# Performance work log

Hardware: AMD Instinct MI355X
Metric: run time of the kernel (lower is better)

Reference implementation:

```python
import jax, jax.numpy as jnp
import numpy as np

B, T, D = 8, 1024, 1024
L = 512          # quantizer_latent_dim
V = 8192         # codebook_size
COMMIT = 0.25
PERP_COEF = 0.1


def _l2norm(v, axis=-1):
    return v * jax.lax.rsqrt(jnp.sum(v * v, axis=axis, keepdims=True) + 1e-12)


def _sq_dist(a, b):
    # ||a||^2 - 2 a.b + ||b||^2, a:[N,L] b:[V,L] -> [N,V]
    a2 = jnp.sum(a * a, axis=1, keepdims=True)
    b2 = jnp.sum(b * b, axis=1)[None, :]
    return a2 - 2.0 * jnp.einsum('nl,vl->nv', a, b) + b2


def setup_inputs() -> dict:
    key = jax.random.key(0)
    ks = jax.random.split(key, 4)
    x = jax.random.normal(ks[0], (B, T, D), dtype=jnp.float32)
    codebook = jax.random.normal(ks[1], (V, D), dtype=jnp.float32)
    W_in = jax.random.normal(ks[2], (D, L), dtype=jnp.float32) * (1.0 / np.sqrt(D))
    b_in = jnp.zeros((L,), dtype=jnp.float32)
    W_code = jax.random.normal(ks[3], (D, L), dtype=jnp.float32) * (1.0 / np.sqrt(D))
    b_code = jnp.zeros((L,), dtype=jnp.float32)
    return {"x": x, "codebook": codebook, "W_in": W_in, "b_in": b_in,
            "W_code": W_code, "b_code": b_code}


def _train_loss(quantized, x):
    e_latent = jnp.mean((jax.lax.stop_gradient(quantized) - x) ** 2) * COMMIT
    q_latent = jnp.mean((quantized - jax.lax.stop_gradient(x)) ** 2)
    return e_latent + q_latent


def reference(x, codebook, W_in, b_in, W_code, b_code):
    xf = x.reshape(-1, D)                                      # [N, D]
    latent_input = _l2norm(xf @ W_in + b_in)                   # [N, L]
    latent_code = _l2norm(codebook @ W_code + b_code)          # [V, L]
    sg_latent_code = jax.lax.stop_gradient(_l2norm(latent_code))
    distances = _sq_dist(latent_input, sg_latent_code).reshape(B, T, V)

    # approx_min_k with aggregate_to_topk (k = top_k_value = 1)
    idx = jax.lax.approx_min_k(distances, k=1, reduction_dimension=-1,
                               aggregate_to_topk=True)[1][..., 0]   # [B, T]
    encodings = jax.nn.one_hot(idx, V, dtype=x.dtype)          # [B, T, V]
    quantized = jnp.einsum('btv,vd->btd', encodings, codebook) # [B, T, D]

    codebook_usage = jnp.sum(jnp.sum(encodings, axis=(0, 1)) > 0) / V

    # train=True path: stop-grad quantized, straight-through estimator
    q_sg = jax.lax.stop_gradient(quantized)
    loss = _train_loss(q_sg, x)
    latent_quantized = q_sg @ W_code + b_code                  # code_to_latent(quantized)
    latent_x = x @ W_in + b_in                                 # input_to_latent(x)
    loss = loss + _train_loss(latent_quantized, latent_x)

    quantized_st = x + jax.lax.stop_gradient(q_sg - x)

    avg_probs = jnp.mean(encodings.reshape(-1, V), axis=0)
    log_perplexity = -jnp.sum(avg_probs * jnp.log(avg_probs + 1e-10))
    perplexity = jnp.exp(log_perplexity)
    loss = loss + PERP_COEF * log_perplexity

    return quantized_st, loss, perplexity, codebook_usage
```

## Files before the change

kernel.cpp:

```cpp
#include <hip/hip_runtime.h>
#include <hip/hip_bf16.h>
#include <stdint.h>

#define NTOK 8192
#define DDIM 1024
#define LDIM 512
#define VCB  8192
#define MROWS 16384

typedef unsigned long long u64;
typedef unsigned short ushort_t;
typedef unsigned char u8;
typedef float f32x4 __attribute__((ext_vector_type(4)));
typedef short s16x8 __attribute__((ext_vector_type(8)));
typedef int i32x8 __attribute__((ext_vector_type(8)));

#define OFF_AB     0ull
#define OFF_QB     0ull
#define OFF_P      ((u64)MROWS * DDIM * 2)
#define OFF_QF     (OFF_P + (u64)MROWS * LDIM * 2)
#define OFF_WT     (OFF_QF + (u64)MROWS * 512)
#define OFF_B2     (OFF_WT + (u64)2 * LDIM * DDIM * 2)
#define OFF_B2B    (OFF_B2 + (u64)VCB * 4)
#define OFF_PART   (OFF_B2B + (u64)VCB * 4)
#define OFF_HIST   (OFF_PART + (u64)NTOK * 64 * 4)
#define OFF_PARTQ  (OFF_HIST + (u64)VCB * 4)
#define OFF_PARTL  (OFF_PARTQ + (u64)NTOK * 4)

__device__ __forceinline__ unsigned key_of(float f) {
  unsigned u = __float_as_uint(f);
  return (u & 0x80000000u) ? ~u : (u | 0x80000000u);
}

__device__ __forceinline__ ushort_t f2bf(float f) {
  unsigned u = __float_as_uint(f);
  unsigned r = (u + 0x7fffu + ((u >> 16) & 1u)) >> 16;
  return (ushort_t)r;
}
__device__ __forceinline__ float bf2f(unsigned b) {
  return __uint_as_float(b << 16);
}
__device__ __forceinline__ unsigned pkbf(float a, float b) {
  __hip_bfloat162 h = __float22bfloat162_rn(make_float2(a, b));
  unsigned r;
  __builtin_memcpy(&r, &h, 4);
  return r;
}

__device__ __forceinline__ void gload_lds16(const void* g, void* l) {
  __builtin_amdgcn_global_load_lds(
      (const __attribute__((address_space(1))) unsigned int*)g,
      (__attribute__((address_space(3))) unsigned int*)l, 16, 0, 0);
}

__device__ __forceinline__ f32x4 mfma16(s16x8 a, s16x8 b, f32x4 c) {
  return __builtin_amdgcn_mfma_f32_16x16x32_bf16(a, b, c, 0, 0, 0);
}
__device__ __forceinline__ f32x4 mfma_mx(i32x8 a, i32x8 b, f32x4 c) {
  return __builtin_amdgcn_mfma_scale_f32_16x16x128_f8f6f4(
      a, b, c, 0, 0, 0, 0x7f7f7f7f, 0, 0x7f7f7f7f);
}

__global__ __launch_bounds__(256)
void k_wt(const float* __restrict__ Wi, const float* __restrict__ Wc,
          ushort_t* __restrict__ Wt, int* __restrict__ hist) {
  __shared__ float tile[32][33];
  const int tx = threadIdx.x, ty = threadIdx.y;
  const int t = ty * 32 + tx;
  const int lb = blockIdx.z * 512 + blockIdx.y * 32 + blockIdx.x;
  if (lb < 32) hist[lb * 256 + t] = 0;
  const float* W = blockIdx.z ? Wc : Wi;
  ushort_t* O = Wt + (blockIdx.z ? (size_t)LDIM * DDIM : 0);
  const int k0 = blockIdx.x * 32, n0 = blockIdx.y * 32;
#pragma unroll
  for (int i = 0; i < 4; ++i)
    tile[ty * 4 + i][tx] = W[(size_t)(k0 + ty * 4 + i) * LDIM + n0 + tx];
  __syncthreads();
#pragma unroll
  for (int i = 0; i < 4; ++i)
    O[(size_t)(n0 + ty * 4 + i) * DDIM + k0 + tx] = f2bf(tile[tx][ty * 4 + i]);
}

__global__ __launch_bounds__(256)
void k_cast(const float* __restrict__ x, const float* __restrict__ cb,
            ushort_t* __restrict__ Ab) {
  size_t i = ((size_t)blockIdx.x * 256 + threadIdx.x) * 8;
  const size_t half = (size_t)NTOK * DDIM;
  const float* src = (i < half) ? (x + i) : (cb + (i - half));
  float4 a = *(const float4*)src;
  float4 b = *(const float4*)(src + 4);
  uint4 o = make_uint4(pkbf(a.x, a.y), pkbf(a.z, a.w),
                       pkbf(b.x, b.y), pkbf(b.z, b.w));
  *(uint4*)&Ab[i] = o;
}

__global__ __launch_bounds__(256)
void k_latent(const ushort_t* __restrict__ Ab, const ushort_t* __restrict__ Wt,
              const float* __restrict__ bi, const float* __restrict__ bc,
              ushort_t* __restrict__ Pb) {
  __shared__ __align__(16) ushort_t As[128 * 32];
  __shared__ __align__(16) ushort_t Bs[128 * 32];
  const int t = threadIdx.x;
  const int wave = t >> 6, lane = t & 63;
  const int col0 = blockIdx.x * 128;
  const int m0 = blockIdx.y * 128;
  const bool isCode = (m0 >= NTOK);
  const u8* A = (const u8*)(Ab + (size_t)m0 * DDIM);
  const u8* W = (const u8*)(Wt + (isCode ? (size_t)LDIM * DDIM : 0) +
                            (size_t)col0 * DDIM);
  const float* bias = isCode ? bc : bi;

  const int srow = lane >> 2;
  const int rA = wave * 16 + srow;
  const int rB = 64 + wave * 16 + srow;
  const size_t goA = (size_t)rA * 2048 +
                     (((lane & 3) ^ (rA & 3) ^ ((rA >> 2) & 3)) << 4);
  const size_t goB = (size_t)rB * 2048 +
                     (((lane & 3) ^ (rB & 3) ^ ((rB >> 2) & 3)) << 4);
  u8* lwA0 = (u8*)As + (wave * 16) * 64;
  u8* lwA1 = (u8*)As + (64 + wave * 16) * 64;
  u8* lwB0 = (u8*)Bs + (wave * 16) * 64;
  u8* lwB1 = (u8*)Bs + (64 + wave * 16) * 64;

  const int wm = wave >> 1, wn = wave & 1;
  const int m = lane & 15, q = lane >> 4;
  const int pq = (q ^ (m & 3) ^ ((m >> 2) & 3)) * 16;
  int roffA[4], roffB[4];
#pragma unroll
  for (int i = 0; i < 4; ++i) {
    roffA[i] = (wm * 64 + i * 16 + m) * 64 + pq;
    roffB[i] = (wn * 64 + i * 16 + m) * 64 + pq;
  }

  f32x4 acc[4][4];
#pragma unroll
  for (int i = 0; i < 4; ++i)
#pragma unroll
    for (int j = 0; j < 4; ++j) acc[i][j] = (f32x4)(0.f);

  for (int it = 0; it < DDIM / 32; ++it) {
    const size_t kb = (size_t)it * 64;
    __syncthreads();
    gload_lds16(A + goA + kb, lwA0);
    gload_lds16(A + goB + kb, lwA1);
    gload_lds16(W + goA + kb, lwB0);
    gload_lds16(W + goB + kb, lwB1);
    __syncthreads();
    s16x8 af[4], bfr[4];
#pragma unroll
    for (int i = 0; i < 4; ++i)
      af[i] = *(const s16x8*)((const u8*)As + roffA[i]);
#pragma unroll
    for (int j = 0; j < 4; ++j)
      bfr[j] = *(const s16x8*)((const u8*)Bs + roffB[j]);
#pragma unroll
    for (int i = 0; i < 4; ++i)
#pragma unroll
      for (int j = 0; j < 4; ++j)
        acc[i][j] = mfma16(af[i], bfr[j], acc[i][j]);
  }

  float bv[4];
#pragma unroll
  for (int j = 0; j < 4; ++j) bv[j] = bias[col0 + wn * 64 + j * 16 + m];
#pragma unroll
  for (int i = 0; i < 4; ++i)
#pragma unroll
    for (int j = 0; j < 4; ++j) {
      int col = col0 + wn * 64 + j * 16 + m;
#pragma unroll
      for (int reg = 0; reg < 4; ++reg) {
        int row = m0 + wm * 64 + i * 16 + q * 4 + reg;
        Pb[(size_t)row * LDIM + col] = f2bf(acc[i][j][reg] + bv[j]);
      }
    }
}

__global__ __launch_bounds__(256)
void k_rownorm(const ushort_t* __restrict__ P, u8* __restrict__ Qf,
               ushort_t* __restrict__ Qb, float* __restrict__ b2,
               float* __restrict__ b2b) {
  const int row = blockIdx.x;
  const int t = threadIdx.x;
  const int lane = t & 63, wid = t >> 6;
  __shared__ float red[4];
  __shared__ float2 red2[4];
  __shared__ float bcast;
  const int k = 2 * t;
  unsigned pv = *(const unsigned*)&P[(size_t)row * LDIM + k];
  float v0 = bf2f(pv & 0xffffu), v1 = bf2f(pv >> 16);
  float s = fmaf(v0, v0, v1 * v1);
#pragma unroll
  for (int o = 32; o > 0; o >>= 1) s += __shfl_down(s, o, 64);
  if (lane == 0) red[wid] = s;
  __syncthreads();
  if (t == 0) {
    float tot = red[0] + red[1] + red[2] + red[3];
    bcast = (float)(1.0 / sqrt((double)tot + 1e-12));
  }
  __syncthreads();
  float rs = bcast;
  int p8 = __builtin_amdgcn_cvt_pk_fp8_f32(v0 * rs, v1 * rs, 0, false);
  ((ushort_t*)Qf)[(size_t)row * 256 + t] = (ushort_t)((unsigned)p8 & 0xFFFFu);
  unsigned qp = pkbf(v0 * rs, v1 * rs);
  *(unsigned*)&Qb[(size_t)row * LDIM + k] = qp;
  if (row >= NTOK) {
    float f0 = __builtin_amdgcn_cvt_f32_fp8(p8, 0);
    float f1 = __builtin_amdgcn_cvt_f32_fp8(p8, 1);
    float g0 = bf2f(qp & 0xffffu), g1 = bf2f(qp >> 16);
    float s8 = fmaf(f0, f0, f1 * f1);
    float sb = fmaf(g0, g0, g1 * g1);
#pragma unroll
    for (int o = 32; o > 0; o >>= 1) {
      s8 += __shfl_down(s8, o, 64);
      sb += __shfl_down(sb, o, 64);
    }
    __syncthreads();
    if (lane == 0) red2[wid] = make_float2(s8, sb);
    __syncthreads();
    if (t == 0) {
      b2[row - NTOK]  = red2[0].x + red2[1].x + red2[2].x + red2[3].x;
      b2b[row - NTOK] = red2[0].y + red2[1].y + red2[2].y + red2[3].y;
    }
  }
}

__global__ __launch_bounds__(256)
void k_dist(const u8* __restrict__ Qf, const float* __restrict__ b2,
            unsigned* __restrict__ part) {
  __shared__ __align__(16) u8 S[2][128 * 128];
  u8* As = S[0];
  u8* Bs = S[1];
  const int t = threadIdx.x;
  const int wave = t >> 6, lane = t & 63;
  const int v0 = blockIdx.x * 128;
  const int n0 = blockIdx.y * 128;
  const u8* Ga = Qf + (size_t)n0 * 512;
  const u8* Gb = Qf + (size_t)(NTOK + v0) * 512;

  const int srow8 = lane >> 3;
  const int sslot = lane & 7;
  size_t go[4];
  u8 *lwA[4], *lwB[4];
#pragma unroll
  for (int p = 0; p < 4; ++p) {
    const int r = wave * 32 + p * 8 + srow8;
    go[p] = (size_t)r * 512 + (size_t)((sslot ^ (r & 7)) << 4);
    lwA[p] = As + (wave * 32 + p * 8) * 128;
    lwB[p] = Bs + (wave * 32 + p * 8) * 128;
  }

  const int wm = wave >> 1, wn = wave & 1;
  const int m = lane & 15, q = lane >> 4;
  int roffA[4][2], roffB[4][2];
#pragma unroll
  for (int i = 0; i < 4; ++i) {
    int fr = wm * 64 + i * 16 + m;
    roffA[i][0] = fr * 128 + (((2 * q) ^ (fr & 7)) << 4);
    roffA[i][1] = fr * 128 + (((2 * q + 1) ^ (fr & 7)) << 4);
    fr = wn * 64 + i * 16 + m;
    roffB[i][0] = fr * 128 + (((2 * q) ^ (fr & 7)) << 4);
    roffB[i][1] = fr * 128 + (((2 * q + 1) ^ (fr & 7)) << 4);
  }

  f32x4 acc[4][4];
#pragma unroll
  for (int i = 0; i < 4; ++i)
#pragma unroll
    for (int j = 0; j < 4; ++j) acc[i][j] = (f32x4)(0.f);

  for (int it = 0; it < 4; ++it) {
    const int k0 = it * 128;
    __syncthreads();
#pragma unroll
    for (int p = 0; p < 4; ++p) gload_lds16(Ga + go[p] + k0, lwA[p]);
#pragma unroll
    for (int p = 0; p < 4; ++p) gload_lds16(Gb + go[p] + k0, lwB[p]);
    __syncthreads();
    i32x8 av[4], bv[4];
#pragma unroll
    for (int i = 0; i < 4; ++i) {
      uint4 lo = *(const uint4*)(As + roffA[i][0]);
      uint4 hi = *(const uint4*)(As + roffA[i][1]);
      av[i][0] = (int)lo.x; av[i][1] = (int)lo.y;
      av[i][2] = (int)lo.z; av[i][3] = (int)lo.w;
      av[i][4] = (int)hi.x; av[i][5] = (int)hi.y;
      av[i][6] = (int)hi.z; av[i][7] = (int)hi.w;
    }
#pragma unroll
    for (int j = 0; j < 4; ++j) {
      uint4 lo = *(const uint4*)(Bs + roffB[j][0]);
      uint4 hi = *(const uint4*)(Bs + roffB[j][1]);
      bv[j][0] = (int)lo.x; bv[j][1] = (int)lo.y;
      bv[j][2] = (int)lo.z; bv[j][3] = (int)lo.w;
      bv[j][4] = (int)hi.x; bv[j][5] = (int)hi.y;
      bv[j][6] = (int)hi.z; bv[j][7] = (int)hi.w;
    }
#pragma unroll
    for (int i = 0; i < 4; ++i)
#pragma unroll
      for (int j = 0; j < 4; ++j)
        acc[i][j] = mfma_mx(av[i], bv[j], acc[i][j]);
  }

  float b2v[4];
#pragma unroll
  for (int j = 0; j < 4; ++j) b2v[j] = b2[v0 + wn * 64 + j * 16 + m];

  __syncthreads();
  unsigned* tbl = (unsigned*)S;
#pragma unroll
  for (int i = 0; i < 4; ++i)
#pragma unroll
    for (int reg = 0; reg < 4; ++reg) {
      unsigned best = 0xFFFFFFFFu;
#pragma unroll
      for (int j = 0; j < 4; ++j) {
        float key = fmaf(-2.f, acc[i][j][reg], b2v[j]);
        unsigned pk = (key_of(key) & 0xFFFFE000u) |
                      (unsigned)(v0 + wn * 64 + j * 16 + m);
        best = (pk < best) ? pk : best;
      }
      int r = wm * 64 + i * 16 + q * 4 + reg;
      int slot = (wn * 16 + m) ^ ((r & 7) << 2);
      tbl[r * 32 + slot] = best;
    }
  __syncthreads();
  if (t < 128) {
    unsigned mn = 0xFFFFFFFFu;
#pragma unroll
    for (int cc = 0; cc < 8; ++cc) {
      int gc = (cc + t) & 7;
      int base = t * 32 + ((gc * 4) ^ ((t & 7) << 2));
      uint4 v = *(const uint4*)&tbl[base];
      unsigned a = (v.x < v.y) ? v.x : v.y;
      unsigned b = (v.z < v.w) ? v.z : v.w;
      a = (a < b) ? a : b;
      mn = (a < mn) ? a : mn;
    }
    part[(size_t)(n0 + t) * 64 + blockIdx.x] = mn;
  }
}

__global__ __launch_bounds__(256)
void k_gather(const unsigned* __restrict__ part, const float* __restrict__ cb,
              const float* __restrict__ x, const ushort_t* __restrict__ P,
              const ushort_t* __restrict__ Qb, const float* __restrict__ b2b,
              float* __restrict__ out, int* __restrict__ hist,
              float* __restrict__ partq, float* __restrict__ partl) {
  const int n = blockIdx.x;
  const int t = threadIdx.x;
  const int lane = t & 63, wid = t >> 6;
  __shared__ float qin[512];
  __shared__ unsigned cand[8];
  __shared__ unsigned wcand[8];
  __shared__ int sIdx;
  __shared__ float rq[4], rl[4];

  unsigned uq = ((const unsigned*)(Qb + (size_t)n * LDIM))[t];
  qin[2 * t] = bf2f(uq & 0xffffu);
  qin[2 * t + 1] = bf2f(uq >> 16);

  if (t < 64) {
    unsigned v = part[(size_t)n * 64 + t];
#pragma unroll
    for (int it = 0; it < 8; ++it) {
      unsigned mn = v;
#pragma unroll
      for (int msk = 1; msk < 64; msk <<= 1) {
        unsigned o = (unsigned)__shfl_xor((int)mn, msk, 64);
        mn = (o < mn) ? o : mn;
      }
      if (t == 0) cand[it] = mn;
      if (v == mn) v = 0xFFFFFFFFu;
    }
  }
  __syncthreads();

  const int c = t >> 5, sl = t & 31;
  const int cidx = (int)(cand[c] & 0x1FFFu);
  const unsigned* crow =
      (const unsigned*)(Qb + (size_t)(NTOK + cidx) * LDIM) + sl * 8;
  uint4 va = *(const uint4*)(crow);
  uint4 vb = *(const uint4*)(crow + 4);
  const float* qs = &qin[sl * 16];
  float dot = 0.f;
  dot = fmaf(bf2f(va.x & 0xffffu), qs[0], dot);
  dot = fmaf(bf2f(va.x >> 16),     qs[1], dot);
  dot = fmaf(bf2f(va.y & 0xffffu), qs[2], dot);
  dot = fmaf(bf2f(va.y >> 16),     qs[3], dot);
  dot = fmaf(bf2f(va.z & 0xffffu), qs[4], dot);
  dot = fmaf(bf2f(va.z >> 16),     qs[5], dot);
  dot = fmaf(bf2f(va.w & 0xffffu), qs[6], dot);
  dot = fmaf(bf2f(va.w >> 16),     qs[7], dot);
  dot = fmaf(bf2f(vb.x & 0xffffu), qs[8], dot);
  dot = fmaf(bf2f(vb.x >> 16),     qs[9], dot);
  dot = fmaf(bf2f(vb.y & 0xffffu), qs[10], dot);
  dot = fmaf(bf2f(vb.y >> 16),     qs[11], dot);
  dot = fmaf(bf2f(vb.z & 0xffffu), qs[12], dot);
  dot = fmaf(bf2f(vb.z >> 16),     qs[13], dot);
  dot = fmaf(bf2f(vb.w & 0xffffu), qs[14], dot);
  dot = fmaf(bf2f(vb.w >> 16),     qs[15], dot);
#pragma unroll
  for (int msk = 1; msk < 32; msk <<= 1) dot += __shfl_xor(dot, msk, 32);
  if (sl == 0) {
    float key = fmaf(-2.f, dot, b2b[cidx]);
    wcand[c] = (key_of(key) & 0xFFFFE000u) | (unsigned)cidx;
  }
  __syncthreads();
  if (t == 0) {
    unsigned mm = wcand[0];
#pragma unroll
    for (int i = 1; i < 8; ++i) mm = (wcand[i] < mm) ? wcand[i] : mm;
    int iv = (int)(mm & 0x1FFFu);
    sIdx = iv;
    atomicAdd(&hist[iv], 1);
  }
  __syncthreads();
  const int iv = sIdx;

  float4 qv = *(const float4*)&cb[(size_t)iv * DDIM + t * 4];
  float4 xv = *(const float4*)&x[(size_t)n * DDIM + t * 4];
  *(float4*)&out[(size_t)n * DDIM + t * 4] = qv;
  float d0 = qv.x - xv.x, d1 = qv.y - xv.y, d2 = qv.z - xv.z, d3 = qv.w - xv.w;
  float sq = d0 * d0 + d1 * d1 + d2 * d2 + d3 * d3;
  unsigned lq = *(const unsigned*)&P[(size_t)(NTOK + iv) * LDIM + t * 2];
  unsigned lx = *(const unsigned*)&P[(size_t)n * LDIM + t * 2];
  float e0 = bf2f(lq & 0xffffu) - bf2f(lx & 0xffffu);
  float e1 = bf2f(lq >> 16) - bf2f(lx >> 16);
  float sl2 = e0 * e0 + e1 * e1;
#pragma unroll
  for (int o = 32; o > 0; o >>= 1) {
    sq += __shfl_down(sq, o, 64);
    sl2 += __shfl_down(sl2, o, 64);
  }
  if (lane == 0) { rq[wid] = sq; rl[wid] = sl2; }
  __syncthreads();
  if (t == 0) {
    partq[n] = rq[0] + rq[1] + rq[2] + rq[3];
    partl[n] = rl[0] + rl[1] + rl[2] + rl[3];
  }
}

__global__ __launch_bounds__(1024)
void k_final(const int* __restrict__ hist, const float* __restrict__ partq,
             const float* __restrict__ partl, float* __restrict__ out) {
  const int t = threadIdx.x;
  const int lane = t & 63, wid = t >> 6;
  float perp = 0.f, usedf = 0.f, sq = 0.f, sl = 0.f;
  for (int v = t; v < VCB; v += 1024) {
    int h = hist[v];
    usedf += (h > 0) ? 1.f : 0.f;
    float p = (float)h * (1.f / (float)NTOK);
    perp -= p * logf(p + 1e-10f);
  }
  for (int n = t; n < NTOK; n += 1024) {
    sq += partq[n];
    sl += partl[n];
  }
#pragma unroll
  for (int o = 32; o > 0; o >>= 1) {
    perp  += __shfl_down(perp, o, 64);
    usedf += __shfl_down(usedf, o, 64);
    sq    += __shfl_down(sq, o, 64);
    sl    += __shfl_down(sl, o, 64);
  }
  __shared__ float red[16][4];
  if (lane == 0) {
    red[wid][0] = perp; red[wid][1] = usedf; red[wid][2] = sq; red[wid][3] = sl;
  }
  __syncthreads();
  if (t == 0) {
    float Pp = 0.f, U = 0.f, SQ = 0.f, SL = 0.f;
    for (int w = 0; w < 16; ++w) {
      Pp += red[w][0]; U += red[w][1]; SQ += red[w][2]; SL += red[w][3];
    }
    float mseq = SQ / (float)((size_t)NTOK * DDIM);
    float msel = SL / (float)((size_t)NTOK * LDIM);
    float loss = 1.25f * mseq + 1.25f * msel + 0.1f * Pp;
    out[(size_t)NTOK * DDIM + 0] = loss;
    out[(size_t)NTOK * DDIM + 1] = expf(Pp);
    out[(size_t)NTOK * DDIM + 2] = U / (float)VCB;
  }
}

extern "C" void kernel_launch(void* const* d_in, const int* in_sizes, int n_in,
                              void* d_out, int out_size, void* d_ws, size_t ws_size,
                              hipStream_t stream) {
  const float* x  = (const float*)d_in[0];
  const float* cb = (const float*)d_in[1];
  const float* Wi = (const float*)d_in[2];
  const float* bi = (const float*)d_in[3];
  const float* Wc = (const float*)d_in[4];
  const float* bc = (const float*)d_in[5];
  float* out = (float*)d_out;
  char* ws = (char*)d_ws;
  ushort_t* Ab   = (ushort_t*)(ws + OFF_AB);
  ushort_t* Qb   = (ushort_t*)(ws + OFF_QB);
  ushort_t* P    = (ushort_t*)(ws + OFF_P);
  u8*       Qf   = (u8*)(ws + OFF_QF);
  ushort_t* Wt   = (ushort_t*)(ws + OFF_WT);
  float*    b2   = (float*)(ws + OFF_B2);
  float*    b2b  = (float*)(ws + OFF_B2B);
  unsigned* part = (unsigned*)(ws + OFF_PART);
  int*      hist = (int*)(ws + OFF_HIST);
  float*    partq = (float*)(ws + OFF_PARTQ);
  float*    partl = (float*)(ws + OFF_PARTL);

  hipLaunchKernelGGL(k_wt, dim3(DDIM / 32, LDIM / 32, 2), dim3(32, 8), 0,
                     stream, Wi, Wc, Wt, hist);
  hipLaunchKernelGGL(k_cast, dim3((MROWS * DDIM) / (256 * 8)), dim3(256), 0,
                     stream, x, cb, Ab);
  hipLaunchKernelGGL(k_latent, dim3(LDIM / 128, MROWS / 128), dim3(256), 0,
                     stream, Ab, Wt, bi, bc, P);
  hipLaunchKernelGGL(k_rownorm, dim3(MROWS), dim3(256), 0, stream, P, Qf, Qb,
                     b2, b2b);
  hipLaunchKernelGGL(k_dist, dim3(VCB / 128, NTOK / 128), dim3(256), 0, stream,
                     Qf, b2, part);
  hipLaunchKernelGGL(k_gather, dim3(NTOK), dim3(256), 0, stream, part, cb, x,
                     P, Qb, b2b, out, hist, partq, partl);
  hipLaunchKernelGGL(k_final, dim3(1), dim3(1024), 0, stream, hist, partq,
                     partl, out);
}
```

Measured before the change: 254.9 us.

## Double-buffer k_dist LDS tiles, shuffle-reduce argmin, and one-wave-per-row rownorm

k_dist now double-buffers its A/B LDS tiles, so the global-to-LDS load for the next K slice is issued while MFMAs run on the current slice. The per-row argmin across 16 lanes now uses xor shuffles instead of a swizzled LDS table. k_rownorm switches from one 256-thread block per row to one wave per row with 16-byte vector loads and no block barriers. The costs are doubled LDS use in k_dist, which may lower occupancy, and a changed fp32 summation order in the norms.

```diff
diff --git a/kernel.cpp b/kernel.cpp
--- a/kernel.cpp
+++ b/kernel.cpp
@@ -60,6 +60,11 @@
   return __builtin_amdgcn_mfma_scale_f32_16x16x128_f8f6f4(
       a, b, c, 0, 0, 0, 0x7f7f7f7f, 0, 0x7f7f7f7f);
 }
+
+__device__ __forceinline__ float fp8_byte_f32_0(int w) { return __builtin_amdgcn_cvt_f32_fp8(w, 0); }
+__device__ __forceinline__ float fp8_byte_f32_1(int w) { return __builtin_amdgcn_cvt_f32_fp8(w, 1); }
+__device__ __forceinline__ float fp8_byte_f32_2(int w) { return __builtin_amdgcn_cvt_f32_fp8(w, 2); }
+__device__ __forceinline__ float fp8_byte_f32_3(int w) { return __builtin_amdgcn_cvt_f32_fp8(w, 3); }
 
 __global__ __launch_bounds__(256)
 void k_wt(const float* __restrict__ Wi, const float* __restrict__ Wc,
@@ -180,47 +185,59 @@
 void k_rownorm(const ushort_t* __restrict__ P, u8* __restrict__ Qf,
                ushort_t* __restrict__ Qb, float* __restrict__ b2,
                float* __restrict__ b2b) {
-  const int row = blockIdx.x;
-  const int t = threadIdx.x;
-  const int lane = t & 63, wid = t >> 6;
-  __shared__ float red[4];
-  __shared__ float2 red2[4];
-  __shared__ float bcast;
-  const int k = 2 * t;
-  unsigned pv = *(const unsigned*)&P[(size_t)row * LDIM + k];
-  float v0 = bf2f(pv & 0xffffu), v1 = bf2f(pv >> 16);
-  float s = fmaf(v0, v0, v1 * v1);
-#pragma unroll
-  for (int o = 32; o > 0; o >>= 1) s += __shfl_down(s, o, 64);
-  if (lane == 0) red[wid] = s;
-  __syncthreads();
-  if (t == 0) {
-    float tot = red[0] + red[1] + red[2] + red[3];
-    bcast = (float)(1.0 / sqrt((double)tot + 1e-12));
-  }
-  __syncthreads();
-  float rs = bcast;
-  int p8 = __builtin_amdgcn_cvt_pk_fp8_f32(v0 * rs, v1 * rs, 0, false);
-  ((ushort_t*)Qf)[(size_t)row * 256 + t] = (ushort_t)((unsigned)p8 & 0xFFFFu);
-  unsigned qp = pkbf(v0 * rs, v1 * rs);
-  *(unsigned*)&Qb[(size_t)row * LDIM + k] = qp;
+  const int row = blockIdx.x * 4 + (threadIdx.x >> 6);
+  const int l = threadIdx.x & 63;
+  const uint4 pv = *(const uint4*)(P + (size_t)row * LDIM + l * 8);
+  float v[8];
+  v[0] = bf2f(pv.x & 0xffffu); v[1] = bf2f(pv.x >> 16);
+  v[2] = bf2f(pv.y & 0xffffu); v[3] = bf2f(pv.y >> 16);
+  v[4] = bf2f(pv.z & 0xffffu); v[5] = bf2f(pv.z >> 16);
+  v[6] = bf2f(pv.w & 0xffffu); v[7] = bf2f(pv.w >> 16);
+  float s = 0.f;
+#pragma unroll
+  for (int k = 0; k < 8; ++k) s = fmaf(v[k], v[k], s);
+#pragma unroll
+  for (int msk = 1; msk < 64; msk <<= 1) s += __shfl_xor(s, msk, 64);
+  const float rs = (float)(1.0 / sqrt((double)s + 1e-12));
+  float w[8];
+#pragma unroll
+  for (int k = 0; k < 8; ++k) w[k] = v[k] * rs;
+  unsigned q0 = (unsigned)__builtin_amdgcn_cvt_pk_fp8_f32(w[0], w[1], 0, false);
+  q0 = (unsigned)__builtin_amdgcn_cvt_pk_fp8_f32(w[2], w[3], (int)q0, true);
+  unsigned q1 = (unsigned)__builtin_amdgcn_cvt_pk_fp8_f32(w[4], w[5], 0, false);
+  q1 = (unsigned)__builtin_amdgcn_cvt_pk_fp8_f32(w[6], w[7], (int)q1, true);
+  *(uint2*)(Qf + (size_t)row * 512 + l * 8) = make_uint2(q0, q1);
+  uint4 qb = make_uint4(pkbf(w[0], w[1]), pkbf(w[2], w[3]),
+                        pkbf(w[4], w[5]), pkbf(w[6], w[7]));
+  *(uint4*)(Qb + (size_t)row * LDIM + l * 8) = qb;
   if (row >= NTOK) {
-    float f0 = __builtin_amdgcn_cvt_f32_fp8(p8, 0);
-    float f1 = __builtin_amdgcn_cvt_f32_fp8(p8, 1);
-    float g0 = bf2f(qp & 0xffffu), g1 = bf2f(qp >> 16);
-    float s8 = fmaf(f0, f0, f1 * f1);
-    float sb = fmaf(g0, g0, g1 * g1);
-#pragma unroll
-    for (int o = 32; o > 0; o >>= 1) {
-      s8 += __shfl_down(s8, o, 64);
-      sb += __shfl_down(sb, o, 64);
-    }
-    __syncthreads();
-    if (lane == 0) red2[wid] = make_float2(s8, sb);
-    __syncthreads();
-    if (t == 0) {
-      b2[row - NTOK]  = red2[0].x + red2[1].x + red2[2].x + red2[3].x;
-      b2b[row - NTOK] = red2[0].y + red2[1].y + red2[2].y + red2[3].y;
+    float s8 = 0.f, sb = 0.f;
+    {
+      float f;
+      f = fp8_byte_f32_0((int)q0); s8 = fmaf(f, f, s8);
+      f = fp8_byte_f32_1((int)q0); s8 = fmaf(f, f, s8);
+      f = fp8_byte_f32_2((int)q0); s8 = fmaf(f, f, s8);
+      f = fp8_byte_f32_3((int)q0); s8 = fmaf(f, f, s8);
+      f = fp8_byte_f32_0((int)q1); s8 = fmaf(f, f, s8);
+      f = fp8_byte_f32_1((int)q1); s8 = fmaf(f, f, s8);
+      f = fp8_byte_f32_2((int)q1); s8 = fmaf(f, f, s8);
+      f = fp8_byte_f32_3((int)q1); s8 = fmaf(f, f, s8);
+    }
+    unsigned qw[4] = {qb.x, qb.y, qb.z, qb.w};
+#pragma unroll
+    for (int i = 0; i < 4; ++i) {
+      float g0 = bf2f(qw[i] & 0xffffu), g1 = bf2f(qw[i] >> 16);
+      sb = fmaf(g0, g0, sb);
+      sb = fmaf(g1, g1, sb);
+    }
+#pragma unroll
+    for (int msk = 1; msk < 64; msk <<= 1) {
+      s8 += __shfl_xor(s8, msk, 64);
+      sb += __shfl_xor(sb, msk, 64);
+    }
+    if (l == 0) {
+      b2[row - NTOK] = s8;
+      b2b[row - NTOK] = sb;
     }
   }
 }
@@ -228,9 +245,7 @@
 __global__ __launch_bounds__(256)
 void k_dist(const u8* __restrict__ Qf, const float* __restrict__ b2,
             unsigned* __restrict__ part) {
-  __shared__ __align__(16) u8 S[2][128 * 128];
-  u8* As = S[0];
-  u8* Bs = S[1];
+  __shared__ __align__(16) u8 S[2][2][128 * 128];
   const int t = threadIdx.x;
   const int wave = t >> 6, lane = t & 63;
   const int v0 = blockIdx.x * 128;
@@ -241,13 +256,12 @@
   const int srow8 = lane >> 3;
   const int sslot = lane & 7;
   size_t go[4];
-  u8 *lwA[4], *lwB[4];
+  int lwo[4];
 #pragma unroll
   for (int p = 0; p < 4; ++p) {
     const int r = wave * 32 + p * 8 + srow8;
     go[p] = (size_t)r * 512 + (size_t)((sslot ^ (r & 7)) << 4);
-    lwA[p] = As + (wave * 32 + p * 8) * 128;
-    lwB[p] = Bs + (wave * 32 + p * 8) * 128;
+    lwo[p] = (wave * 32 + p * 8) * 128;
   }
 
   const int wm = wave >> 1, wn = wave & 1;
@@ -269,14 +283,25 @@
 #pragma unroll
     for (int j = 0; j < 4; ++j) acc[i][j] = (f32x4)(0.f);
 
+#pragma unroll
+  for (int p = 0; p < 4; ++p) gload_lds16(Ga + go[p], &S[0][0][lwo[p]]);
+#pragma unroll
+  for (int p = 0; p < 4; ++p) gload_lds16(Gb + go[p], &S[0][1][lwo[p]]);
+  __syncthreads();
+
+#pragma unroll
   for (int it = 0; it < 4; ++it) {
-    const int k0 = it * 128;
-    __syncthreads();
-#pragma unroll
-    for (int p = 0; p < 4; ++p) gload_lds16(Ga + go[p] + k0, lwA[p]);
-#pragma unroll
-    for (int p = 0; p < 4; ++p) gload_lds16(Gb + go[p] + k0, lwB[p]);
-    __syncthreads();
+    const int cur = it & 1, nxt = (it + 1) & 1;
+    if (it < 3) {
+      const int k0 = (it + 1) * 128;
+#pragma unroll
+      for (int p = 0; p < 4; ++p) gload_lds16(Ga + go[p] + k0, &S[nxt][0][lwo[p]]);
+#pragma unroll
+      for (int p = 0; p < 4; ++p) gload_lds16(Gb + go[p] + k0, &S[nxt][1][lwo[p]]);
+    }
+    __builtin_amdgcn_sched_barrier(0);
+    const u8* As = S[cur][0];
+    const u8* Bs = S[cur][1];
     i32x8 av[4], bv[4];
 #pragma unroll
     for (int i = 0; i < 4; ++i) {
@@ -301,14 +326,14 @@
 #pragma unroll
       for (int j = 0; j < 4; ++j)
         acc[i][j] = mfma_mx(av[i], bv[j], acc[i][j]);
+    __syncthreads();
   }
 
   float b2v[4];
 #pragma unroll
   for (int j = 0; j < 4; ++j) b2v[j] = b2[v0 + wn * 64 + j * 16 + m];
 
-  __syncthreads();
-  unsigned* tbl = (unsigned*)S;
+  unsigned* halfA = (unsigned*)S;
 #pragma unroll
   for (int i = 0; i < 4; ++i)
 #pragma unroll
@@ -321,24 +346,20 @@
                       (unsigned)(v0 + wn * 64 + j * 16 + m);
         best = (pk < best) ? pk : best;
       }
-      int r = wm * 64 + i * 16 + q * 4 + reg;
-      int slot = (wn * 16 + m) ^ ((r & 7) << 2);
-      tbl[r * 32 + slot] = best;
+#pragma unroll
+      for (int msk = 1; msk < 16; msk <<= 1) {
+        unsigned o = (unsigned)__shfl_xor((int)best, msk, 64);
+        best = (o < best) ? o : best;
+      }
+      if (m == 0) {
+        int r = wm * 64 + i * 16 + q * 4 + reg;
+        halfA[wn * 128 + r] = best;
+      }
     }
   __syncthreads();
   if (t < 128) {
-    unsigned mn = 0xFFFFFFFFu;
-#pragma unroll
-    for (int cc = 0; cc < 8; ++cc) {
-      int gc = (cc + t) & 7;
-      int base = t * 32 + ((gc * 4) ^ ((t & 7) << 2));
-      uint4 v = *(const uint4*)&tbl[base];
-      unsigned a = (v.x < v.y) ? v.x : v.y;
-      unsigned b = (v.z < v.w) ? v.z : v.w;
-      a = (a < b) ? a : b;
-      mn = (a < mn) ? a : mn;
-    }
-    part[(size_t)(n0 + t) * 64 + blockIdx.x] = mn;
+    unsigned a = halfA[t], b = halfA[128 + t];
+    part[(size_t)(n0 + t) * 64 + blockIdx.x] = (a < b) ? a : b;
   }
 }
 
@@ -513,8 +534,8 @@
                      stream, x, cb, Ab);
   hipLaunchKernelGGL(k_latent, dim3(LDIM / 128, MROWS / 128), dim3(256), 0,
                      stream, Ab, Wt, bi, bc, P);
-  hipLaunchKernelGGL(k_rownorm, dim3(MROWS), dim3(256), 0, stream, P, Qf, Qb,
-                     b2, b2b);
+  hipLaunchKernelGGL(k_rownorm, dim3(MROWS / 4), dim3(256), 0, stream, P, Qf,
+                     Qb, b2, b2b);
   hipLaunchKernelGGL(k_dist, dim3(VCB / 128, NTOK / 128), dim3(256), 0, stream,
                      Qf, b2, part);
   hipLaunchKernelGGL(k_gather, dim3(NTOK), dim3(256), 0, stream, part, cb, x,
```

New measurement: 313.6 us. 1.23x slower.
